# Optimization experiments

Hardware: AMD Instinct MI355X
Metric: run time of the kernel (lower is better)

The kernel has to match this reference:

```python
import jax, jax.numpy as jnp
import numpy as np
from jax import lax

B, L, P, CIN, N, HD, PH, K = 2048, 96, 96, 8, 64, 64, 8, 3
DIM_C = CIN * N  # 512


def _silu(x):
    return x * jax.nn.sigmoid(x)


def _lin(x, w, b):
    return x @ w.T + b


def setup_inputs() -> dict:
    key = jax.random.key(0)
    ks = iter(jax.random.split(key, 64))

    def w(shape):
        fan_in = shape[-1]
        return (jax.random.normal(next(ks), shape, jnp.float32) / np.sqrt(fan_in)).astype(jnp.float32)

    inp = {"x": jax.random.normal(next(ks), (B, L, CIN), jnp.float32)}
    # x_proj: 5 Linears (enc_in->h, h->h, h->h, h->h, h->N), SiLU between (dropout=eval/identity)
    inp["xp_w0"] = w((HD, CIN)); inp["xp_b0"] = jnp.zeros((HD,), jnp.float32)
    inp["xp_w1"] = w((HD, HD));  inp["xp_b1"] = jnp.zeros((HD,), jnp.float32)
    inp["xp_w2"] = w((HD, HD));  inp["xp_b2"] = jnp.zeros((HD,), jnp.float32)
    inp["xp_w3"] = w((HD, HD));  inp["xp_b3"] = jnp.zeros((HD,), jnp.float32)
    inp["xp_w4"] = w((N, HD));   inp["xp_b4"] = jnp.zeros((N,), jnp.float32)
    # x_proj_: Linear(N,h), SiLU, Linear(h,N)
    inp["xpp_w0"] = w((HD, N)); inp["xpp_b0"] = jnp.zeros((HD,), jnp.float32)
    inp["xpp_w1"] = w((N, HD)); inp["xpp_b1"] = jnp.zeros((N,), jnp.float32)
    # depthwise dilated Conv1d: weight (N, 1, K)
    inp["conv_w"] = w((N, 1, K)); inp["conv_b"] = jnp.zeros((N,), jnp.float32)
    inp["span_A"] = jnp.asarray(0.1, jnp.float32)
    # compress: Linear(N*L, PH)
    inp["comp_w"] = w((PH, N * L)); inp["comp_b"] = jnp.zeros((PH,), jnp.float32)
    # a_ode.net: Linear(PH,h), SiLU, Linear(h,PH), Tanh
    inp["net_w0"] = w((HD, PH)); inp["net_b0"] = jnp.zeros((HD,), jnp.float32)
    inp["net_w1"] = w((PH, HD)); inp["net_b1"] = jnp.zeros((PH,), jnp.float32)
    # lat2out: Linear(PH,8), SiLU, Linear(8,N)
    inp["lo_w0"] = w((8, PH)); inp["lo_b0"] = jnp.zeros((8,), jnp.float32)
    inp["lo_w1"] = w((N, 8));  inp["lo_b1"] = jnp.zeros((N,), jnp.float32)
    # lat2out_c: Linear(PH,8), SiLU, Linear(8, CIN*N)
    inp["lc_w0"] = w((8, PH));     inp["lc_b0"] = jnp.zeros((8,), jnp.float32)
    inp["lc_w1"] = w((DIM_C, 8));  inp["lc_b1"] = jnp.zeros((DIM_C,), jnp.float32)
    # lat2out_z: Linear(N,N), SiLU, Linear(N, CIN)
    inp["lz_w0"] = w((N, N));   inp["lz_b0"] = jnp.zeros((N,), jnp.float32)
    inp["lz_w1"] = w((CIN, N)); inp["lz_b1"] = jnp.zeros((CIN,), jnp.float32)
    return inp


def reference(x, xp_w0, xp_b0, xp_w1, xp_b1, xp_w2, xp_b2, xp_w3, xp_b3, xp_w4, xp_b4,
              xpp_w0, xpp_b0, xpp_w1, xpp_b1, conv_w, conv_b, span_A, comp_w, comp_b,
              net_w0, net_b0, net_w1, net_b1, lo_w0, lo_b0, lo_w1, lo_b1,
              lc_w0, lc_b0, lc_w1, lc_b1, lz_w0, lz_b0, lz_w1, lz_b1):
    Bsz = x.shape[0]

    def x_proj(t):
        h = _silu(_lin(t, xp_w0, xp_b0))
        h = _silu(_lin(h, xp_w1, xp_b1))
        h = _silu(_lin(h, xp_w2, xp_b2))
        h = _silu(_lin(h, xp_w3, xp_b3))
        return _lin(h, xp_w4, xp_b4)

    x_old = x_proj(x[:, :L])                       # (B, L, N)
    hist = x_old.transpose(0, 2, 1)                # (B, N, L)
    pad = (K - 1) * 2                              # 4
    conv = lax.conv_general_dilated(
        hist, conv_w, window_strides=(1,), padding=[(pad, pad)],
        rhs_dilation=(2,), dimension_numbers=("NCH", "OIH", "NCH"),
        feature_group_count=N) + conv_b[None, :, None]
    hist = _silu(conv)[:, :, -L:]                  # (B, N, L)
    hist_f = hist.transpose(0, 2, 1).reshape(Bsz, L * N)
    vector_F = _lin(hist_f, comp_w, comp_b)        # (B, PH)

    a0 = vector_F
    z0 = x_proj(x[:, L - 1])                       # (B, N)

    # Householder matrix H = I - 2 v v^T with v = normalize(x_proj_(z0))
    v = _lin(_silu(_lin(z0, xpp_w0, xpp_b0)), xpp_w1, xpp_b1)
    v = v / (jnp.linalg.norm(v, axis=-1, keepdims=True) + 1e-8)
    Hh = jnp.eye(N, dtype=x.dtype)[None] - 2.0 * v[:, :, None] * v[:, None, :]  # (B,N,N)

    dt = jnp.clip(span_A, 1e-8, 7.0)               # uniform Euler step size
    s0 = jnp.concatenate([a0, z0], axis=-1)        # (B, PH+N)

    def step(s, _):
        a = s[:, :PH]
        z = s[:, PH:]
        da = jnp.tanh(_lin(_silu(_lin(a, net_w0, net_b0)), net_w1, net_b1))  # (B,PH)
        d = _lin(_silu(_lin(a, lo_w0, lo_b0)), lo_w1, lo_b1)                 # (B,N)
        # dz = H^T diag(d) H z   (fused; avoids materializing A_mat)
        Hz = jnp.einsum('bjk,bk->bj', Hh, z)
        dz = jnp.einsum('bj,bji->bi', d * Hz, Hh)
        s_new = s + dt * jnp.concatenate([da, dz], axis=-1)
        return s_new, s_new

    _, sol = lax.scan(step, s0, None, length=P)    # (P, B, PH+N) == sol[1:]

    c_traj = sol[:, :, :PH]                        # (P, B, PH)
    z_traj = sol[:, :, PH:]                        # (P, B, N)

    C = _lin(_silu(_lin(c_traj, lc_w0, lc_b0)), lc_w1, lc_b1)  # (P, B, CIN*N)
    C = C.reshape(P, Bsz, CIN, N)
    y_hat_c = jnp.einsum('pbcn,pbn->pbc', C, z_traj)           # (P, B, CIN)
    added_z = _lin(_silu(_lin(z_traj, lz_w0, lz_b0)), lz_w1, lz_b1)
    x_pred = (y_hat_c + added_z).transpose(1, 0, 2)            # (B, P, CIN)

    x_rec = x[:, :L, :]
    return (x_rec, x_pred)
```

## Files before the change

kernel.cpp:

```cpp
#include <hip/hip_runtime.h>
#include <cstdint>
#include <cstddef>

#define BB 2048
#define LL 96
#define PP 96
#define NN 64
#define HSTRIDE 68

typedef __attribute__((ext_vector_type(8))) short short8;
typedef __attribute__((ext_vector_type(4))) float f32x4;

union U4S8 { uint4 u; short8 s; };

__device__ __forceinline__ float siluf(float x) {
  return x * __builtin_amdgcn_rcpf(1.0f + __expf(-x));
}
__device__ __forceinline__ float tanhf_fast(float x) {
  return 1.0f - 2.0f * __builtin_amdgcn_rcpf(1.0f + __expf(2.0f * x));
}
__device__ __forceinline__ float rlane(float x, int l) {
  return __int_as_float(__builtin_amdgcn_readlane(__float_as_int(x), l));
}

template <int CTRL>
__device__ __forceinline__ float dppadd(float x) {
  int y = __builtin_amdgcn_update_dpp(0, __float_as_int(x), CTRL, 0xF, 0xF, false);
  return x + __int_as_float(y);
}
template <int CTRL>
__device__ __forceinline__ float dppmov(float x) {
  int y = __builtin_amdgcn_update_dpp(0, __float_as_int(x), CTRL, 0xF, 0xF, false);
  return __int_as_float(y);
}
template <int IMM>
__device__ __forceinline__ float swzf(float x) {
  return __int_as_float(__builtin_amdgcn_ds_swizzle(__float_as_int(x), IMM));
}
__device__ __forceinline__ float wave_sum(float x) {
  x = dppadd<0xB1>(x);
  x = dppadd<0x4E>(x);
  x = dppadd<0x141>(x);
  x = dppadd<0x128>(x);
  x += __shfl_xor(x, 16, 64);
  x += __shfl_xor(x, 32, 64);
  return x;
}

__device__ __forceinline__ uint32_t packsplit(float f) {
  uint32_t b = __float_as_uint(f);
  uint32_t h = b & 0xFFFF0000u;
  float r = f - __uint_as_float(h);
  return h | (__float_as_uint(r) >> 16);
}
__device__ __forceinline__ void splitpack2(float f0, float f1, uint32_t& dhi, uint32_t& dlo) {
  uint32_t b0 = __float_as_uint(f0), b1 = __float_as_uint(f1);
  uint32_t h0 = b0 & 0xFFFF0000u, h1 = b1 & 0xFFFF0000u;
  float r0 = f0 - __uint_as_float(h0), r1 = f1 - __uint_as_float(h1);
  dhi = (h0 >> 16) | h1;
  dlo = (__float_as_uint(r0) >> 16) | (__float_as_uint(r1) & 0xFFFF0000u);
}
__device__ __forceinline__ void unpack2(uint32_t p0, uint32_t p1, uint32_t& dhi, uint32_t& dlo) {
  dhi = (p0 >> 16) | (p1 & 0xFFFF0000u);
  dlo = (p0 & 0xFFFFu) | (p1 << 16);
}
__device__ __forceinline__ void readfrag(const uint32_t* p, short8& hi, short8& lo) {
  uint4 pa = *(const uint4*)p;
  uint4 pb = *(const uint4*)(p + 4);
  U4S8 h, l;
  unpack2(pa.x, pa.y, h.u.x, l.u.x);
  unpack2(pa.z, pa.w, h.u.y, l.u.y);
  unpack2(pb.x, pb.y, h.u.z, l.u.z);
  unpack2(pb.z, pb.w, h.u.w, l.u.w);
  hi = h.s; lo = l.s;
}
__device__ __forceinline__ f32x4 mm_split(f32x4 acc, const short8* Ah, const short8* Al,
                                          const short8* Bh, const short8* Bl) {
  acc = __builtin_amdgcn_mfma_f32_16x16x32_bf16(Ah[0], Bh[0], acc, 0, 0, 0);
  acc = __builtin_amdgcn_mfma_f32_16x16x32_bf16(Ah[1], Bh[1], acc, 0, 0, 0);
  acc = __builtin_amdgcn_mfma_f32_16x16x32_bf16(Al[0], Bh[0], acc, 0, 0, 0);
  acc = __builtin_amdgcn_mfma_f32_16x16x32_bf16(Al[1], Bh[1], acc, 0, 0, 0);
  acc = __builtin_amdgcn_mfma_f32_16x16x32_bf16(Ah[0], Bl[0], acc, 0, 0, 0);
  acc = __builtin_amdgcn_mfma_f32_16x16x32_bf16(Ah[1], Bl[1], acc, 0, 0, 0);
  return acc;
}

__global__ __launch_bounds__(256, 2) void k_xproj(
    const float* __restrict__ x,
    const float* __restrict__ w0, const float* __restrict__ b0,
    const float* __restrict__ w1, const float* __restrict__ b1,
    const float* __restrict__ w2, const float* __restrict__ b2,
    const float* __restrict__ w3, const float* __restrict__ b3,
    const float* __restrict__ w4, const float* __restrict__ b4,
    float* __restrict__ x_old, float* __restrict__ out)
{
  __shared__ uint32_t hbuf[128 * HSTRIDE];
  __shared__ uint32_t wbufA[64 * HSTRIDE];
  __shared__ uint32_t wbufB[64 * HSTRIDE];
  __shared__ float bs[320];

  int tid = threadIdx.x;
  int wave = tid >> 6, lane = tid & 63;
  int quad = lane >> 4, m16 = lane & 15;
  size_t tokBase = (size_t)blockIdx.x * 128;

  {
    size_t e = tokBase * 8 + (size_t)tid * 4;
    *(float4*)(out + e) = *(const float4*)(x + e);
  }
  if (tid < 64) {
    bs[tid]       = b0[tid];
    bs[64 + tid]  = b1[tid];
    bs[128 + tid] = b2[tid];
    bs[192 + tid] = b3[tid];
    bs[256 + tid] = b4[tid];
  }
  #pragma unroll
  for (int i = 0; i < 4; ++i) {
    int e4 = i * 256 + tid;
    int o = e4 >> 4, k = (e4 & 15) << 2;
    float4 wv = ((const float4*)w1)[e4];
    *(uint4*)(wbufA + o * HSTRIDE + k) =
        make_uint4(packsplit(wv.x), packsplit(wv.y), packsplit(wv.z), packsplit(wv.w));
  }
  __syncthreads();

  short8 A0h[2], A0l[2];
  #pragma unroll
  for (int mt = 0; mt < 2; ++mt) {
    U4S8 h, l;
    h.u = make_uint4(0, 0, 0, 0); l.u = make_uint4(0, 0, 0, 0);
    if (quad == 0) {
      const float* xp = x + (tokBase + wave * 32 + mt * 16 + m16) * 8;
      float4 xa = *(const float4*)xp;
      float4 xb = *(const float4*)(xp + 4);
      splitpack2(xa.x, xa.y, h.u.x, l.u.x);
      splitpack2(xa.z, xa.w, h.u.y, l.u.y);
      splitpack2(xb.x, xb.y, h.u.z, l.u.z);
      splitpack2(xb.z, xb.w, h.u.w, l.u.w);
    }
    A0h[mt] = h.s; A0l[mt] = l.s;
  }
  short8 B0h[4], B0l[4];
  #pragma unroll
  for (int nt = 0; nt < 4; ++nt) {
    U4S8 h, l;
    h.u = make_uint4(0, 0, 0, 0); l.u = make_uint4(0, 0, 0, 0);
    if (quad == 0) {
      const float* wp = w0 + (nt * 16 + m16) * 8;
      float4 wa = *(const float4*)wp;
      float4 wb = *(const float4*)(wp + 4);
      splitpack2(wa.x, wa.y, h.u.x, l.u.x);
      splitpack2(wa.z, wa.w, h.u.y, l.u.y);
      splitpack2(wb.x, wb.y, h.u.z, l.u.z);
      splitpack2(wb.z, wb.w, h.u.w, l.u.w);
    }
    B0h[nt] = h.s; B0l[nt] = l.s;
  }
  {
    f32x4 acc[2][4];
    #pragma unroll
    for (int mt = 0; mt < 2; ++mt)
      #pragma unroll
      for (int nt = 0; nt < 4; ++nt) {
        float bv = bs[nt * 16 + m16];
        acc[mt][nt] = (f32x4){bv, bv, bv, bv};
      }
    #pragma unroll
    for (int mt = 0; mt < 2; ++mt)
      #pragma unroll
      for (int nt = 0; nt < 4; ++nt)
        acc[mt][nt] = __builtin_amdgcn_mfma_f32_16x16x32_bf16(A0h[mt], B0h[nt], acc[mt][nt], 0, 0, 0);
    #pragma unroll
    for (int mt = 0; mt < 2; ++mt)
      #pragma unroll
      for (int nt = 0; nt < 4; ++nt)
        acc[mt][nt] = __builtin_amdgcn_mfma_f32_16x16x32_bf16(A0l[mt], B0h[nt], acc[mt][nt], 0, 0, 0);
    #pragma unroll
    for (int mt = 0; mt < 2; ++mt)
      #pragma unroll
      for (int nt = 0; nt < 4; ++nt)
        acc[mt][nt] = __builtin_amdgcn_mfma_f32_16x16x32_bf16(A0h[mt], B0l[nt], acc[mt][nt], 0, 0, 0);
    #pragma unroll
    for (int mt = 0; mt < 2; ++mt)
      #pragma unroll
      for (int nt = 0; nt < 4; ++nt)
        #pragma unroll
        for (int r = 0; r < 4; ++r) {
          float s = siluf(acc[mt][nt][r]);
          hbuf[(wave * 32 + mt * 16 + quad * 4 + r) * HSTRIDE + nt * 16 + m16] = packsplit(s);
        }
  }

  const float* Ws[4] = {w1, w2, w3, w4};
  uint32_t* cur = wbufA;
  uint32_t* nxt = wbufB;
  #pragma unroll 1
  for (int lyr = 0; lyr < 4; ++lyr) {
    float4 wv[4];
    if (lyr < 3) {
      const float* wn = Ws[lyr + 1];
      #pragma unroll
      for (int i = 0; i < 4; ++i) wv[i] = ((const float4*)wn)[i * 256 + tid];
    }
    short8 Bh[8], Bl[8];
    #pragma unroll
    for (int nt = 0; nt < 4; ++nt)
      #pragma unroll
      for (int ks = 0; ks < 2; ++ks)
        readfrag(cur + (nt * 16 + m16) * HSTRIDE + ks * 32 + quad * 8, Bh[nt * 2 + ks], Bl[nt * 2 + ks]);
    short8 Ah[4], Al[4];
    #pragma unroll
    for (int mt = 0; mt < 2; ++mt)
      #pragma unroll
      for (int ks = 0; ks < 2; ++ks)
        readfrag(hbuf + (wave * 32 + mt * 16 + m16) * HSTRIDE + ks * 32 + quad * 8, Ah[mt * 2 + ks], Al[mt * 2 + ks]);

    f32x4 acc[2][4];
    #pragma unroll
    for (int mt = 0; mt < 2; ++mt)
      #pragma unroll
      for (int nt = 0; nt < 4; ++nt) {
        float bv = bs[(lyr + 1) * 64 + nt * 16 + m16];
        acc[mt][nt] = (f32x4){bv, bv, bv, bv};
      }
    #pragma unroll
    for (int ks = 0; ks < 2; ++ks)
      #pragma unroll
      for (int mt = 0; mt < 2; ++mt)
        #pragma unroll
        for (int nt = 0; nt < 4; ++nt)
          acc[mt][nt] = __builtin_amdgcn_mfma_f32_16x16x32_bf16(Ah[mt * 2 + ks], Bh[nt * 2 + ks], acc[mt][nt], 0, 0, 0);
    #pragma unroll
    for (int ks = 0; ks < 2; ++ks)
      #pragma unroll
      for (int mt = 0; mt < 2; ++mt)
        #pragma unroll
        for (int nt = 0; nt < 4; ++nt)
          acc[mt][nt] = __builtin_amdgcn_mfma_f32_16x16x32_bf16(Al[mt * 2 + ks], Bh[nt * 2 + ks], acc[mt][nt], 0, 0, 0);
    #pragma unroll
    for (int ks = 0; ks < 2; ++ks)
      #pragma unroll
      for (int mt = 0; mt < 2; ++mt)
        #pragma unroll
        for (int nt = 0; nt < 4; ++nt)
          acc[mt][nt] = __builtin_amdgcn_mfma_f32_16x16x32_bf16(Ah[mt * 2 + ks], Bl[nt * 2 + ks], acc[mt][nt], 0, 0, 0);

    if (lyr < 3) {
      #pragma unroll
      for (int i = 0; i < 4; ++i) {
        int e4 = i * 256 + tid;
        int o = e4 >> 4, k = (e4 & 15) << 2;
        *(uint4*)(nxt + o * HSTRIDE + k) =
            make_uint4(packsplit(wv[i].x), packsplit(wv[i].y), packsplit(wv[i].z), packsplit(wv[i].w));
      }
    }

    if (lyr < 3) {
      #pragma unroll
      for (int mt = 0; mt < 2; ++mt)
        #pragma unroll
        for (int nt = 0; nt < 4; ++nt)
          #pragma unroll
          for (int r = 0; r < 4; ++r) {
            float s = siluf(acc[mt][nt][r]);
            hbuf[(wave * 32 + mt * 16 + quad * 4 + r) * HSTRIDE + nt * 16 + m16] = packsplit(s);
          }
    } else {
      #pragma unroll
      for (int mt = 0; mt < 2; ++mt)
        #pragma unroll
        for (int nt = 0; nt < 4; ++nt)
          #pragma unroll
          for (int r = 0; r < 4; ++r) {
            size_t t = tokBase + wave * 32 + mt * 16 + quad * 4 + r;
            x_old[t * 64 + nt * 16 + m16] = acc[mt][nt][r];
          }
    }
    __syncthreads();
    uint32_t* tmp = cur; cur = nxt; nxt = tmp;
  }
}

__global__ __launch_bounds__(256) void k_hist(
    const float* __restrict__ x_old,
    const float* __restrict__ conv_w, const float* __restrict__ conv_b,
    const float* __restrict__ comp_w, const float* __restrict__ comp_b,
    const float* __restrict__ xw0, const float* __restrict__ xb0,
    const float* __restrict__ xw1, const float* __restrict__ xb1,
    float* __restrict__ a0_o, float* __restrict__ v_o, float* __restrict__ z0_o)
{
  __shared__ float xo[LL * NN];
  __shared__ float red[32];
  __shared__ float hbuf[64];
  int b = blockIdx.x, tid = threadIdx.x;
  const float* src = x_old + (size_t)b * (LL * NN);
  #pragma unroll
  for (int i = 0; i < 6; ++i) {
    int e = (i * 256 + tid) * 4;
    *(float4*)(xo + e) = *(const float4*)(src + e);
  }
  __syncthreads();
  int c = tid & 63;
  float cw0 = conv_w[c * 3], cw1 = conv_w[c * 3 + 1], cw2 = conv_w[c * 3 + 2];
  float cb = conv_b[c];
  float acc[8];
  #pragma unroll
  for (int q = 0; q < 8; ++q) acc[q] = 0.f;
  #pragma unroll 1
  for (int j = 0; j < 24; ++j) {
    int e = j * 256 + tid;
    int t = e >> 6;
    float s = xo[t * 64 + c] * cw0 + cb;
    if (t + 2 < LL) s += xo[(t + 2) * 64 + c] * cw1;
    if (t + 4 < LL) s += xo[(t + 4) * 64 + c] * cw2;
    float hv = siluf(s);
    #pragma unroll
    for (int q = 0; q < 8; ++q) acc[q] += hv * comp_w[q * 6144 + e];
  }
  #pragma unroll
  for (int q = 0; q < 8; ++q) acc[q] = dppadd<0xB1>(acc[q]);
  #pragma unroll
  for (int q = 0; q < 8; ++q) acc[q] = dppadd<0x4E>(acc[q]);
  #pragma unroll
  for (int q = 0; q < 8; ++q) acc[q] = dppadd<0x141>(acc[q]);
  #pragma unroll
  for (int q = 0; q < 8; ++q) acc[q] = dppadd<0x128>(acc[q]);
  #pragma unroll
  for (int q = 0; q < 8; ++q) acc[q] += __shfl_xor(acc[q], 16, 64);
  #pragma unroll
  for (int q = 0; q < 8; ++q) acc[q] += __shfl_xor(acc[q], 32, 64);
  int wave = tid >> 6, lane = tid & 63;
  if (lane < 8) {
    float sel = acc[0];
    #pragma unroll
    for (int q = 1; q < 8; ++q) sel = (lane == q) ? acc[q] : sel;
    red[wave * 8 + lane] = sel;
  }
  __syncthreads();
  if (tid < 8)
    a0_o[b * 8 + tid] = red[tid] + red[8 + tid] + red[16 + tid] + red[24 + tid] + comp_b[tid];
  if (tid < 64) {
    float a2 = xb0[tid];
    #pragma unroll 8
    for (int k = 0; k < 64; ++k) a2 += xw0[tid * 64 + k] * xo[6080 + k];
    hbuf[tid] = siluf(a2);
  }
  __syncthreads();
  float vr = 0.f;
  if (tid < 64) {
    vr = xb1[tid];
    #pragma unroll 8
    for (int k = 0; k < 64; ++k) vr += xw1[tid * 64 + k] * hbuf[k];
  }
  float s2 = wave_sum(vr * vr);
  if (tid < 64) {
    float nrm = sqrtf(s2) + 1e-8f;
    v_o[b * 64 + tid] = vr / nrm;
    z0_o[b * 64 + tid] = xo[6080 + tid];
  }
}

__global__ __launch_bounds__(256) void k_scan(
    const float* __restrict__ a0_i, const float* __restrict__ v_i, const float* __restrict__ z0_i,
    const float* __restrict__ nw0, const float* __restrict__ nb0_p,
    const float* __restrict__ nw1, const float* __restrict__ nb1_p,
    const float* __restrict__ lw0, const float* __restrict__ lb0_p,
    const float* __restrict__ lw1, const float* __restrict__ lb1_p,
    const float* __restrict__ spanA, float* __restrict__ atraj, uint32_t* __restrict__ ztraj)
{
  int tid = threadIdx.x;
  int lane = tid & 63;
  int wv = tid >> 6;
  int b = blockIdx.x * 4 + wv;
  float dt = fminf(fmaxf(spanA[0], 1e-8f), 7.0f);
  int i8 = lane & 7;
  int oct = lane >> 3;

  float w0r[8], wx[8], g0r[8], d1r[8];
  #pragma unroll
  for (int i = 0; i < 8; ++i) w0r[i] = nw0[lane * 8 + i];
  #pragma unroll
  for (int m = 0; m < 8; ++m) wx[m] = nw1[i8 * 64 + oct * 8 + (i8 ^ m)];
  #pragma unroll
  for (int i = 0; i < 8; ++i) g0r[i] = lw0[i8 * 8 + i];
  #pragma unroll
  for (int i = 0; i < 8; ++i) d1r[i] = lw1[lane * 8 + i];
  float nb0 = nb0_p[lane];
  float nb1o = nb1_p[i8];
  float lb0o = lb0_p[i8];
  float lb1 = lb1_p[lane];
  float v = v_i[b * 64 + lane];
  float z = z0_i[b * 64 + lane];
  float a_own = a0_i[b * 8 + i8];
  float t0 = wave_sum(v * z);
  float w = z - 2.0f * t0 * v;
  float a_s[8];
  #pragma unroll
  for (int i = 0; i < 8; ++i) a_s[i] = rlane(a_own, i);

  float* ab = atraj + (size_t)b * (PP * 8);
  uint32_t* zb = ztraj + (size_t)b * (PP * NN);
  #pragma unroll 1
  for (int p = 0; p < PP; ++p) {
    float u0 = w0r[0] * a_s[0] + w0r[1] * a_s[1];
    float u1 = w0r[2] * a_s[2] + w0r[3] * a_s[3];
    float u2 = w0r[4] * a_s[4] + w0r[5] * a_s[5];
    float u3 = w0r[6] * a_s[6] + w0r[7] * a_s[7];
    float h = siluf(nb0 + ((u0 + u1) + (u2 + u3)));
    float v1 = dppmov<0xB1>(h);
    float v2 = dppmov<0x4E>(h);
    float v3 = dppmov<0x1B>(h);
    float v7 = dppmov<0x141>(h);
    float v4 = swzf<0x101F>(h);
    float v5 = swzf<0x101F>(v1);
    float v6 = swzf<0x101F>(v2);
    float q0 = wx[0] * h  + wx[1] * v1;
    float q1 = wx[2] * v2 + wx[3] * v3;
    float q2 = wx[4] * v4 + wx[5] * v5;
    float q3 = wx[6] * v6 + wx[7] * v7;
    float ps = (q0 + q1) + (q2 + q3);
    ps += swzf<0x201F>(ps);
    ps += swzf<0x401F>(ps);
    ps += __shfl_xor(ps, 32, 64);
    float da_own = tanhf_fast(ps + nb1o);
    float e0 = g0r[0] * a_s[0] + g0r[1] * a_s[1];
    float e1 = g0r[2] * a_s[2] + g0r[3] * a_s[3];
    float e2 = g0r[4] * a_s[4] + g0r[5] * a_s[5];
    float e3 = g0r[6] * a_s[6] + g0r[7] * a_s[7];
    float g_own = siluf(lb0o + ((e0 + e1) + (e2 + e3)));
    float f0 = d1r[0] * rlane(g_own, 0) + d1r[1] * rlane(g_own, 1);
    float f1 = d1r[2] * rlane(g_own, 2) + d1r[3] * rlane(g_own, 3);
    float f2 = d1r[4] * rlane(g_own, 4) + d1r[5] * rlane(g_own, 5);
    float f3 = d1r[6] * rlane(g_own, 6) + d1r[7] * rlane(g_own, 7);
    float d = lb1 + ((f0 + f1) + (f2 + f3));
    a_own += dt * da_own;
    #pragma unroll
    for (int i = 0; i < 8; ++i) a_s[i] = rlane(a_own, i);
    w *= (1.0f + dt * d);
    float t1 = wave_sum(v * w);
    float zv = w - 2.0f * t1 * v;
    if (lane < 8) ab[p * 8 + lane] = a_own;
    zb[p * 64 + lane] = packsplit(zv);
  }
}

__global__ __launch_bounds__(256, 4) void k_post(
    const float* __restrict__ atraj, const uint32_t* __restrict__ ztraj,
    const float* __restrict__ cw0, const float* __restrict__ cb0,
    const float* __restrict__ cw1, const float* __restrict__ cb1,
    const float* __restrict__ zw0, const float* __restrict__ zb0,
    const float* __restrict__ zw1, const float* __restrict__ zb1,
    float* __restrict__ out)
{
  __shared__ uint32_t wbuf[144 * HSTRIDE];
  __shared__ float    cw0s[64];
  __shared__ float    cb0s[8];
  __shared__ float    zb0s[64];
  __shared__ float    zb1s[8];

  int tid = threadIdx.x;
  int wave = tid >> 6, lane = tid & 63;
  int quad = lane >> 4, m16 = lane & 15;
  size_t tokBase = (size_t)blockIdx.x * 64;

  #pragma unroll
  for (int i = 0; i < 36; ++i) {
    int e = i * 256 + tid;
    int o = e >> 6, k = e & 63;
    float wv;
    if (o < 64)       wv = cw1[(((o >> 3) * 64 + k) << 3) + (o & 7)];
    else if (o < 72)  wv = cb1[(o - 64) * 64 + k];
    else if (o < 136) wv = zw0[(o - 72) * 64 + k];
    else              wv = zw1[(o - 136) * 64 + k];
    wbuf[o * HSTRIDE + k] = packsplit(wv);
  }
  if (tid < 64) cw0s[tid] = cw0[tid];
  if (tid < 8)  cb0s[tid] = cb0[tid];
  if (tid < 64) zb0s[tid] = zb0[tid];
  if (tid < 8)  zb1s[tid] = zb1[tid];
  __syncthreads();

  const uint32_t* zp = ztraj + (tokBase + wave * 16 + m16) * 64;
  short8 Ah[2], Al[2];
  readfrag(zp + quad * 8,      Ah[0], Al[0]);
  readfrag(zp + 32 + quad * 8, Ah[1], Al[1]);

  f32x4 acc1[5];
  #pragma unroll
  for (int nt = 0; nt < 5; ++nt) {
    short8 Bh[2], Bl[2];
    readfrag(wbuf + (nt * 16 + m16) * HSTRIDE + quad * 8,      Bh[0], Bl[0]);
    readfrag(wbuf + (nt * 16 + m16) * HSTRIDE + 32 + quad * 8, Bh[1], Bl[1]);
    f32x4 acc = (f32x4){0.f, 0.f, 0.f, 0.f};
    acc1[nt] = mm_split(acc, Ah, Al, Bh, Bl);
  }
  __syncthreads();

  uint32_t* ebuf = wbuf;
  #pragma unroll
  for (int nt = 0; nt < 4; ++nt) {
    short8 Bh[2], Bl[2];
    readfrag(wbuf + (72 + nt * 16 + m16) * HSTRIDE + quad * 8,      Bh[0], Bl[0]);
    readfrag(wbuf + (72 + nt * 16 + m16) * HSTRIDE + 32 + quad * 8, Bh[1], Bl[1]);
    f32x4 acc = (f32x4){0.f, 0.f, 0.f, 0.f};
    acc = mm_split(acc, Ah, Al, Bh, Bl);
    int m = nt * 16 + m16;
    float zbv = zb0s[m];
    #pragma unroll
    for (int r = 0; r < 4; ++r) {
      float e = siluf(acc[r] + zbv);
      ebuf[(wave * 16 + quad * 4 + r) * HSTRIDE + m] = packsplit(e);
    }
  }

  f32x4 acc3;
  {
    short8 Eh[2], El[2];
    readfrag(ebuf + (wave * 16 + m16) * HSTRIDE + quad * 8,      Eh[0], El[0]);
    readfrag(ebuf + (wave * 16 + m16) * HSTRIDE + 32 + quad * 8, Eh[1], El[1]);
    short8 Bh[2], Bl[2];
    int brow = 136 + (m16 & 7);
    readfrag(wbuf + brow * HSTRIDE + quad * 8,      Bh[0], Bl[0]);
    readfrag(wbuf + brow * HSTRIDE + 32 + quad * 8, Bh[1], Bl[1]);
    f32x4 acc = (f32x4){0.f, 0.f, 0.f, 0.f};
    acc3 = mm_split(acc, Eh, El, Bh, Bl);
  }

  int j = m16 & 7;
  float cwj[8];
  #pragma unroll
  for (int i = 0; i < 8; ++i) cwj[i] = cw0s[j * 8 + i];
  float cbj = cb0s[j];
  #pragma unroll
  for (int r = 0; r < 4; ++r) {
    size_t idx = tokBase + wave * 16 + quad * 4 + r;
    const float* ap = atraj + idx * 8;
    float4 a0v = *(const float4*)ap;
    float4 a1v = *(const float4*)(ap + 4);
    float g2v = cbj
      + cwj[0] * a0v.x + cwj[1] * a0v.y + cwj[2] * a0v.z + cwj[3] * a0v.w
      + cwj[4] * a1v.x + cwj[5] * a1v.y + cwj[6] * a1v.z + cwj[7] * a1v.w;
    g2v = siluf(g2v);
    float yc[4], qo[4];
    #pragma unroll
    for (int nt = 0; nt < 4; ++nt) {
      float p = acc1[nt][r] * g2v;
      p = dppadd<0xB1>(p);
      p = dppadd<0x4E>(p);
      p = dppadd<0x141>(p);
      yc[nt] = p;
      qo[nt] = dppmov<0x128>(p);
    }
    if (m16 < 8) {
      int cc = m16;
      int nt = cc >> 1;
      float ye = (nt == 0) ? yc[0] : (nt == 1) ? yc[1] : (nt == 2) ? yc[2] : yc[3];
      float yo = (nt == 0) ? qo[0] : (nt == 1) ? qo[1] : (nt == 2) ? qo[2] : qo[3];
      float y = (cc & 1) ? yo : ye;
      y += acc1[4][r] + acc3[r] + zb1s[cc];
      out[(size_t)(BB * LL * 8) + idx * 8 + cc] = y;
    }
  }
}

extern "C" void kernel_launch(void* const* d_in, const int* in_sizes, int n_in,
                              void* d_out, int out_size, void* d_ws, size_t ws_size,
                              hipStream_t stream) {
  const float* x      = (const float*)d_in[0];
  const float* xp_w0  = (const float*)d_in[1];
  const float* xp_b0  = (const float*)d_in[2];
  const float* xp_w1  = (const float*)d_in[3];
  const float* xp_b1  = (const float*)d_in[4];
  const float* xp_w2  = (const float*)d_in[5];
  const float* xp_b2  = (const float*)d_in[6];
  const float* xp_w3  = (const float*)d_in[7];
  const float* xp_b3  = (const float*)d_in[8];
  const float* xp_w4  = (const float*)d_in[9];
  const float* xp_b4  = (const float*)d_in[10];
  const float* xpp_w0 = (const float*)d_in[11];
  const float* xpp_b0 = (const float*)d_in[12];
  const float* xpp_w1 = (const float*)d_in[13];
  const float* xpp_b1 = (const float*)d_in[14];
  const float* conv_w = (const float*)d_in[15];
  const float* conv_b = (const float*)d_in[16];
  const float* span_A = (const float*)d_in[17];
  const float* comp_w = (const float*)d_in[18];
  const float* comp_b = (const float*)d_in[19];
  const float* net_w0 = (const float*)d_in[20];
  const float* net_b0 = (const float*)d_in[21];
  const float* net_w1 = (const float*)d_in[22];
  const float* net_b1 = (const float*)d_in[23];
  const float* lo_w0  = (const float*)d_in[24];
  const float* lo_b0  = (const float*)d_in[25];
  const float* lo_w1  = (const float*)d_in[26];
  const float* lo_b1  = (const float*)d_in[27];
  const float* lc_w0  = (const float*)d_in[28];
  const float* lc_b0  = (const float*)d_in[29];
  const float* lc_w1  = (const float*)d_in[30];
  const float* lc_b1  = (const float*)d_in[31];
  const float* lz_w0  = (const float*)d_in[32];
  const float* lz_b0  = (const float*)d_in[33];
  const float* lz_w1  = (const float*)d_in[34];
  const float* lz_b1  = (const float*)d_in[35];

  float*    ws    = (float*)d_ws;
  float*    x_old = ws;
  uint32_t* ztraj = (uint32_t*)ws;
  float*    atraj = ws + 12582912;
  float*    a0    = ws + 14155776;
  float*    vv    = a0 + 2048 * 8;
  float*    z0    = vv + 2048 * 64;
  float*    out   = (float*)d_out;

  hipLaunchKernelGGL(k_xproj, dim3(1536), dim3(256), 0, stream,
                     x, xp_w0, xp_b0, xp_w1, xp_b1, xp_w2, xp_b2, xp_w3, xp_b3,
                     xp_w4, xp_b4, x_old, out);
  hipLaunchKernelGGL(k_hist, dim3(2048), dim3(256), 0, stream,
                     x_old, conv_w, conv_b, comp_w, comp_b,
                     xpp_w0, xpp_b0, xpp_w1, xpp_b1, a0, vv, z0);
  hipLaunchKernelGGL(k_scan, dim3(512), dim3(256), 0, stream,
                     a0, vv, z0, net_w0, net_b0, net_w1, net_b1,
                     lo_w0, lo_b0, lo_w1, lo_b1, span_A, atraj, ztraj);
  hipLaunchKernelGGL(k_post, dim3(3072), dim3(256), 0, stream,
                     atraj, ztraj, lc_w0, lc_b0, lc_w1, lc_b1,
                     lz_w0, lz_b0, lz_w1, lz_b1, out);
}
```

Baseline: 311.8 us.

## Use permlane swaps for cross-row reductions and software-pipeline scan output

Result: faster. 303.7 us (-2.6%).

```diff
diff --git a/kernel.cpp b/kernel.cpp
--- a/kernel.cpp
+++ b/kernel.cpp
@@ -33,17 +33,39 @@
   int y = __builtin_amdgcn_update_dpp(0, __float_as_int(x), CTRL, 0xF, 0xF, false);
   return __int_as_float(y);
 }
-template <int IMM>
-__device__ __forceinline__ float swzf(float x) {
-  return __int_as_float(__builtin_amdgcn_ds_swizzle(__float_as_int(x), IMM));
-}
+
+__device__ __forceinline__ float addswap16(float x) {
+#if __has_builtin(__builtin_amdgcn_permlane16_swap)
+  auto r = __builtin_amdgcn_permlane16_swap(__float_as_uint(x), __float_as_uint(x), false, false);
+  return __uint_as_float(r[0]) + __uint_as_float(r[1]);
+#else
+  return x + __shfl_xor(x, 16, 64);
+#endif
+}
+__device__ __forceinline__ float addswap32(float x) {
+#if __has_builtin(__builtin_amdgcn_permlane32_swap)
+  auto r = __builtin_amdgcn_permlane32_swap(__float_as_uint(x), __float_as_uint(x), false, false);
+  return __uint_as_float(r[0]) + __uint_as_float(r[1]);
+#else
+  return x + __shfl_xor(x, 32, 64);
+#endif
+}
+__device__ __forceinline__ float movswap32(float x, bool hi) {
+#if __has_builtin(__builtin_amdgcn_permlane32_swap)
+  auto r = __builtin_amdgcn_permlane32_swap(__float_as_uint(x), __float_as_uint(x), false, false);
+  return __uint_as_float(hi ? r[0] : r[1]);
+#else
+  return __shfl_xor(x, 32, 64);
+#endif
+}
+
 __device__ __forceinline__ float wave_sum(float x) {
   x = dppadd<0xB1>(x);
   x = dppadd<0x4E>(x);
   x = dppadd<0x141>(x);
   x = dppadd<0x128>(x);
-  x += __shfl_xor(x, 16, 64);
-  x += __shfl_xor(x, 32, 64);
+  x = addswap16(x);
+  x = addswap32(x);
   return x;
 }
 
@@ -327,9 +349,9 @@
   #pragma unroll
   for (int q = 0; q < 8; ++q) acc[q] = dppadd<0x128>(acc[q]);
   #pragma unroll
-  for (int q = 0; q < 8; ++q) acc[q] += __shfl_xor(acc[q], 16, 64);
-  #pragma unroll
-  for (int q = 0; q < 8; ++q) acc[q] += __shfl_xor(acc[q], 32, 64);
+  for (int q = 0; q < 8; ++q) acc[q] = addswap16(acc[q]);
+  #pragma unroll
+  for (int q = 0; q < 8; ++q) acc[q] = addswap32(acc[q]);
   int wave = tid >> 6, lane = tid & 63;
   if (lane < 8) {
     float sel = acc[0];
@@ -375,55 +397,55 @@
   int b = blockIdx.x * 4 + wv;
   float dt = fminf(fmaxf(spanA[0], 1e-8f), 7.0f);
   int i8 = lane & 7;
-  int oct = lane >> 3;
-
-  float w0r[8], wx[8], g0r[8], d1r[8];
+  bool hi32 = lane >= 32;
+  int rrow = ((lane ^ (lane >> 1)) & 1) | (((lane ^ (lane >> 2)) & 1) << 1) | (((lane >> 5) & 1) << 2);
+
+  float w0r[8], wxl[4], wxp[4], g0r[8], d1r[8];
   #pragma unroll
   for (int i = 0; i < 8; ++i) w0r[i] = nw0[lane * 8 + i];
   #pragma unroll
-  for (int m = 0; m < 8; ++m) wx[m] = nw1[i8 * 64 + oct * 8 + (i8 ^ m)];
+  for (int j = 0; j < 4; ++j) wxl[j] = nw1[rrow * 64 + (lane ^ j)];
+  #pragma unroll
+  for (int j = 0; j < 4; ++j) wxp[j] = nw1[(rrow ^ 4) * 64 + (lane ^ j)];
   #pragma unroll
   for (int i = 0; i < 8; ++i) g0r[i] = lw0[i8 * 8 + i];
   #pragma unroll
   for (int i = 0; i < 8; ++i) d1r[i] = lw1[lane * 8 + i];
   float nb0 = nb0_p[lane];
-  float nb1o = nb1_p[i8];
+  float nb1r = nb1_p[rrow];
   float lb0o = lb0_p[i8];
   float lb1 = lb1_p[lane];
   float v = v_i[b * 64 + lane];
   float z = z0_i[b * 64 + lane];
-  float a_own = a0_i[b * 8 + i8];
+  float a_own = a0_i[b * 8 + rrow];
   float t0 = wave_sum(v * z);
   float w = z - 2.0f * t0 * v;
   float a_s[8];
-  #pragma unroll
-  for (int i = 0; i < 8; ++i) a_s[i] = rlane(a_own, i);
+  a_s[0] = rlane(a_own, 0);  a_s[1] = rlane(a_own, 2);
+  a_s[2] = rlane(a_own, 4);  a_s[3] = rlane(a_own, 6);
+  a_s[4] = rlane(a_own, 32); a_s[5] = rlane(a_own, 34);
+  a_s[6] = rlane(a_own, 36); a_s[7] = rlane(a_own, 38);
 
   float* ab = atraj + (size_t)b * (PP * 8);
   uint32_t* zb = ztraj + (size_t)b * (PP * NN);
-  #pragma unroll 1
-  for (int p = 0; p < PP; ++p) {
+  bool astore = (lane & 0x19) == 0;
+
+  auto step_rec = [&]() {
     float u0 = w0r[0] * a_s[0] + w0r[1] * a_s[1];
     float u1 = w0r[2] * a_s[2] + w0r[3] * a_s[3];
     float u2 = w0r[4] * a_s[4] + w0r[5] * a_s[5];
     float u3 = w0r[6] * a_s[6] + w0r[7] * a_s[7];
     float h = siluf(nb0 + ((u0 + u1) + (u2 + u3)));
-    float v1 = dppmov<0xB1>(h);
-    float v2 = dppmov<0x4E>(h);
-    float v3 = dppmov<0x1B>(h);
-    float v7 = dppmov<0x141>(h);
-    float v4 = swzf<0x101F>(h);
-    float v5 = swzf<0x101F>(v1);
-    float v6 = swzf<0x101F>(v2);
-    float q0 = wx[0] * h  + wx[1] * v1;
-    float q1 = wx[2] * v2 + wx[3] * v3;
-    float q2 = wx[4] * v4 + wx[5] * v5;
-    float q3 = wx[6] * v6 + wx[7] * v7;
-    float ps = (q0 + q1) + (q2 + q3);
-    ps += swzf<0x201F>(ps);
-    ps += swzf<0x401F>(ps);
-    ps += __shfl_xor(ps, 32, 64);
-    float da_own = tanhf_fast(ps + nb1o);
+    float hv1 = dppmov<0xB1>(h);
+    float hv2 = dppmov<0x4E>(h);
+    float hv3 = dppmov<0x1B>(h);
+    float slo = (wxl[0] * h + wxl[1] * hv1) + (wxl[2] * hv2 + wxl[3] * hv3);
+    float pre = (wxp[0] * h + wxp[1] * hv1) + (wxp[2] * hv2 + wxp[3] * hv3);
+    float ps = slo + movswap32(pre, hi32);
+    ps = dppadd<0x141>(ps);
+    ps = dppadd<0x128>(ps);
+    ps = addswap16(ps);
+    float da = tanhf_fast(ps + nb1r);
     float e0 = g0r[0] * a_s[0] + g0r[1] * a_s[1];
     float e1 = g0r[2] * a_s[2] + g0r[3] * a_s[3];
     float e2 = g0r[4] * a_s[4] + g0r[5] * a_s[5];
@@ -434,14 +456,31 @@
     float f2 = d1r[4] * rlane(g_own, 4) + d1r[5] * rlane(g_own, 5);
     float f3 = d1r[6] * rlane(g_own, 6) + d1r[7] * rlane(g_own, 7);
     float d = lb1 + ((f0 + f1) + (f2 + f3));
-    a_own += dt * da_own;
-    #pragma unroll
-    for (int i = 0; i < 8; ++i) a_s[i] = rlane(a_own, i);
+    a_own += dt * da;
+    a_s[0] = rlane(a_own, 0);  a_s[1] = rlane(a_own, 2);
+    a_s[2] = rlane(a_own, 4);  a_s[3] = rlane(a_own, 6);
+    a_s[4] = rlane(a_own, 32); a_s[5] = rlane(a_own, 34);
+    a_s[6] = rlane(a_own, 36); a_s[7] = rlane(a_own, 38);
     w *= (1.0f + dt * d);
-    float t1 = wave_sum(v * w);
-    float zv = w - 2.0f * t1 * v;
-    if (lane < 8) ab[p * 8 + lane] = a_own;
-    zb[p * 64 + lane] = packsplit(zv);
+  };
+
+  step_rec();
+  float wo = w, ao = a_own;
+  #pragma unroll 1
+  for (int p = 1; p < PP; ++p) {
+    float woc = wo, aoc = ao;
+    step_rec();
+    wo = w; ao = a_own;
+    float t1 = wave_sum(v * woc);
+    float zv = woc - 2.0f * t1 * v;
+    if (astore) ab[(p - 1) * 8 + rrow] = aoc;
+    zb[(p - 1) * 64 + lane] = packsplit(zv);
+  }
+  {
+    float t1 = wave_sum(v * wo);
+    float zv = wo - 2.0f * t1 * v;
+    if (astore) ab[(PP - 1) * 8 + rrow] = ao;
+    zb[(PP - 1) * 64 + lane] = packsplit(zv);
   }
 }
 
```
